# Performance work log

Measured on AMD Instinct MI355X. Metric: run time of the kernel, lower is better.

The kernel has to match this reference:

```python
import jax, jax.numpy as jnp
import numpy as np

N, C, H, W = 64, 64, 8, 8   # batch, channels (img_net_out_dim), feature-map HxW
E = 256                      # ques_rnn_hidden_dim
G = 512                      # rn_g_dim
FD = 512                     # rn_f_dim
GIN = 2 * (C + 2) + E        # g-MLP input dim = 388
NUM_CLASSES = 2


def _lin(key, din, dout):
    # kaiming-uniform-like init for a Linear stored as (in, out)
    bound = float(np.sqrt(6.0 / din))
    w = jax.random.uniform(key, (din, dout), minval=-bound, maxval=bound, dtype=jnp.float32)
    b = jnp.zeros((dout,), dtype=jnp.float32)
    return w, b


def setup_inputs() -> dict:
    key = jax.random.key(0)
    ks = jax.random.split(key, 9)
    img = jax.random.normal(ks[0], (N, C, H, W), dtype=jnp.float32)
    ques = jax.random.normal(ks[1], (N, E), dtype=jnp.float32)
    g_w1, g_b1 = _lin(ks[2], GIN, G)
    g_w2, g_b2 = _lin(ks[3], G, G)
    g_w3, g_b3 = _lin(ks[4], G, G)
    g_w4, g_b4 = _lin(ks[5], G, G)
    f_w1, f_b1 = _lin(ks[6], G, FD)
    f_w2, f_b2 = _lin(ks[7], FD, FD)
    f_w3, f_b3 = _lin(ks[8], FD, NUM_CLASSES)
    return dict(img=img, ques=ques,
                g_w1=g_w1, g_b1=g_b1, g_w2=g_w2, g_b2=g_b2,
                g_w3=g_w3, g_b3=g_b3, g_w4=g_w4, g_b4=g_b4,
                f_w1=f_w1, f_b1=f_b1, f_w2=f_w2, f_b2=f_b2,
                f_w3=f_w3, f_b3=f_b3)


def _img_to_pairs(img, ques):
    # img: (n, c, h, w), ques: (n, e) -> pairs: (n, hw*hw, 2*(c+2)+e)
    n, c, h, w = img.shape
    hw = h * w
    cells = img.reshape(n, c, hw)
    idx = jnp.arange(hw)
    loc = jnp.stack([idx // w, idx % w], axis=0).astype(img.dtype)  # (2, hw)
    cells = jnp.concatenate([cells, jnp.broadcast_to(loc[None], (n, 2, hw))], axis=1)
    feats = cells.transpose(0, 2, 1)  # (n, hw, c+2)
    fdim = feats.shape[-1]
    one = jnp.broadcast_to(feats[:, :, None, :], (n, hw, hw, fdim))   # object i
    two = jnp.broadcast_to(feats[:, None, :, :], (n, hw, hw, fdim))   # object j
    q = jnp.broadcast_to(ques[:, None, None, :], (n, hw, hw, ques.shape[-1]))
    return jnp.concatenate([one, two, q], axis=-1).reshape(n, hw * hw, -1)


def reference(img, ques, g_w1, g_b1, g_w2, g_b2, g_w3, g_b3, g_w4, g_b4,
              f_w1, f_b1, f_w2, f_b2, f_w3, f_b3):
    pairs = _img_to_pairs(img, ques)                      # (N, HW^2, GIN)
    hdd = jax.nn.relu(pairs @ g_w1 + g_b1)                # shared g-MLP over all pairs
    hdd = jax.nn.relu(hdd @ g_w2 + g_b2)
    hdd = jax.nn.relu(hdd @ g_w3 + g_b3)
    hdd = jax.nn.relu(hdd @ g_w4 + g_b4)
    context = hdd.mean(axis=1)                            # (N, G)
    z = jax.nn.relu(context @ f_w1 + f_b1)                # f-MLP (dropout = identity in eval)
    z = jax.nn.relu(z @ f_w2 + f_b2)
    scores = z @ f_w3 + f_b3                              # (N, 2)
    return jax.nn.log_softmax(scores, axis=1)
```

## Files before the change

### kernel.cpp

```cpp
#include <hip/hip_runtime.h>

typedef unsigned short u16;
typedef unsigned int u32;
typedef _Float16 f16;

using half8 = __attribute__((ext_vector_type(8))) _Float16;
using f32x4 = __attribute__((ext_vector_type(4))) float;
using f32x16 = __attribute__((ext_vector_type(16))) float;

__global__ __launch_bounds__(512) void prep_p12(const float* __restrict__ img,
                                                const float* __restrict__ gw1,
                                                float* __restrict__ P1,
                                                f16* __restrict__ P2h) {
    const int blk = blockIdx.x;
    const int n = blk >> 3;
    const int c0 = (blk & 7) * 8;
    const int t = threadIdx.x;
    __shared__ float feats[8][68];
    for (int idx = t; idx < 8 * 66; idx += 512) {
        int rr = idx / 66, cc = idx % 66, cell = c0 + rr;
        float v;
        if (cc < 64)       v = img[((size_t)(n * 64 + cc)) * 64 + cell];
        else if (cc == 64) v = (float)(cell >> 3);
        else               v = (float)(cell & 7);
        feats[rr][cc] = v;
    }
    __syncthreads();
    const int g = t;
    float a1[8], a2[8];
#pragma unroll
    for (int r = 0; r < 8; ++r) { a1[r] = 0.f; a2[r] = 0.f; }
    for (int c = 0; c < 66; ++c) {
        float wa = gw1[(size_t)c * 512 + g];
        float wb = gw1[(size_t)(66 + c) * 512 + g];
#pragma unroll
        for (int r = 0; r < 8; ++r) {
            a1[r] += feats[r][c] * wa;
            a2[r] += feats[r][c] * wb;
        }
    }
#pragma unroll
    for (int r = 0; r < 8; ++r) {
        P1[((size_t)(n * 64 + c0 + r)) * 512 + g] = a1[r];
        P2h[((size_t)(n * 64 + c0 + r)) * 512 + g] = (f16)a2[r];
    }
}

__global__ __launch_bounds__(512) void prep_q2(const float* __restrict__ ques,
                                               const float* __restrict__ gw1,
                                               const float* __restrict__ gb1,
                                               const float* __restrict__ P1,
                                               f16* __restrict__ P1h,
                                               float* __restrict__ Ctx) {
    const int n = blockIdx.x;
    const int t = threadIdx.x;
    __shared__ float q[256];
    if (t < 256) q[t] = ques[(size_t)n * 256 + t];
    __syncthreads();
    float acc = gb1[t];
    for (int e = 0; e < 256; ++e)
        acc += q[e] * gw1[(size_t)(132 + e) * 512 + t];
    const float* src = P1 + (((size_t)(n * 64)) << 9) + t;
    f16* dst = P1h + (((size_t)(n * 64)) << 9) + t;
    for (int r = 0; r < 64; ++r)
        dst[(size_t)r * 512] = (f16)(src[(size_t)r * 512] + acc);
    Ctx[(size_t)n * 512 + t] = 0.f;
}

__global__ void transpose_w(const float* __restrict__ W2, const float* __restrict__ W3,
                            const float* __restrict__ W4, f16* __restrict__ T2,
                            f16* __restrict__ T3, f16* __restrict__ T4) {
    const int L = blockIdx.z;
    const float* W = (L == 0) ? W2 : ((L == 1) ? W3 : W4);
    f16* T = (L == 0) ? T2 : ((L == 1) ? T3 : T4);
    __shared__ float tile[32][33];
    const int bx = blockIdx.x * 32;
    const int by = blockIdx.y * 32;
    const int tx = threadIdx.x, ty = threadIdx.y;
    for (int r = ty; r < 32; r += 8)
        tile[r][tx] = W[(size_t)(by + r) * 512 + bx + tx];
    __syncthreads();
    for (int r = ty; r < 32; r += 8)
        T[(size_t)(bx + r) * 512 + by + tx] = (f16)tile[tx][r];
}

__global__ __launch_bounds__(512, 2) void fused_g234(
    const f16* __restrict__ P1h, const f16* __restrict__ P2h,
    const f16* __restrict__ T2, const f16* __restrict__ T3,
    const f16* __restrict__ T4, const float* __restrict__ gb2,
    const float* __restrict__ gb3, const float* __restrict__ gb4,
    float* __restrict__ Ctx) {
    const int tid = threadIdx.x;
    const int lane = tid & 63;
    const int lane31 = lane & 31;
    const int khalf = lane >> 5;
    const int wv = tid >> 6;
    const int b = blockIdx.x;
    const int nb = b >> 5;
    const int i0 = (b & 31) * 2;

    __shared__ alignas(16) f16 H[128 * 512];

    const f16* P1b = P1h + (((size_t)(nb * 64 + i0)) << 9);
    const f16* P2b = P2h + (((size_t)(nb * 64)) << 9);

    {
        const int k0 = lane * 8;
#pragma unroll
        for (int u = 0; u < 16; ++u) {
            int r = u * 8 + wv;
            half8 x = *(const half8*)(P1b + (((size_t)(r >> 6)) << 9) + k0);
            half8 y = *(const half8*)(P2b + (((size_t)(r & 63)) << 9) + k0);
            half8 s = x + y;
            s = __builtin_elementwise_max(s, (half8)(f16)0.f);
            *(half8*)&H[r * 512 + (k0 ^ ((wv & 7) << 3))] = s;
        }
    }
    __syncthreads();

    f32x16 acc[4][2];
#pragma unroll
    for (int mi = 0; mi < 4; ++mi)
#pragma unroll
        for (int ni = 0; ni < 2; ++ni)
#pragma unroll
            for (int r = 0; r < 16; ++r)
                acc[mi][ni][r] = 0.f;

    auto loadB = [&](const f16* __restrict__ T, int ks, int ni) -> half8 {
        int col = wv * 64 + ni * 32 + lane31;
        return *(const half8*)(T + (((size_t)col) << 9) + ks * 16 + khalf * 8);
    };

    const int swz = (lane31 & 7) << 3;

    auto run_layer = [&](const f16* __restrict__ T) {
        half8 bfn[2];
#pragma unroll
        for (int ni = 0; ni < 2; ++ni) bfn[ni] = loadB(T, 0, ni);
#pragma unroll 4
        for (int ks = 0; ks < 32; ++ks) {
            half8 bf[2];
#pragma unroll
            for (int ni = 0; ni < 2; ++ni) bf[ni] = bfn[ni];
#pragma unroll
            for (int ni = 0; ni < 2; ++ni) bfn[ni] = loadB(T, (ks + 1) & 31, ni);
            const int koff = (ks * 16 + khalf * 8) ^ swz;
            half8 af[4];
#pragma unroll
            for (int mi = 0; mi < 4; ++mi)
                af[mi] = *(const half8*)&H[(mi * 32 + lane31) * 512 + koff];
#pragma unroll
            for (int mi = 0; mi < 4; ++mi)
#pragma unroll
                for (int ni = 0; ni < 2; ++ni)
                    acc[mi][ni] = __builtin_amdgcn_mfma_f32_32x32x16_f16(
                        af[mi], bf[ni], acc[mi][ni], 0, 0, 0);
        }
    };

    auto writeback = [&](const float* __restrict__ bias) {
        float bb[2];
#pragma unroll
        for (int ni = 0; ni < 2; ++ni)
            bb[ni] = bias[wv * 64 + ni * 32 + lane31];
        __syncthreads();
#pragma unroll
        for (int mi = 0; mi < 4; ++mi) {
#pragma unroll
            for (int ni = 0; ni < 2; ++ni) {
                int col = wv * 64 + ni * 32 + lane31;
#pragma unroll
                for (int r = 0; r < 16; ++r) {
                    int row = mi * 32 + (r & 3) + 4 * khalf + 8 * (r >> 2);
                    float v = fmaxf(acc[mi][ni][r] + bb[ni], 0.f);
                    H[row * 512 + (col ^ ((row & 7) << 3))] = (f16)v;
                    acc[mi][ni][r] = 0.f;
                }
            }
        }
        __syncthreads();
    };

    run_layer(T2);
    writeback(gb2);
    run_layer(T3);
    writeback(gb3);
    run_layer(T4);

#pragma unroll
    for (int ni = 0; ni < 2; ++ni) {
        int col = wv * 64 + ni * 32 + lane31;
        float bb = gb4[col];
        float s = 0.f;
#pragma unroll
        for (int mi = 0; mi < 4; ++mi)
#pragma unroll
            for (int r = 0; r < 16; ++r)
                s += fmaxf(acc[mi][ni][r] + bb, 0.f);
        s += __shfl_xor(s, 32, 64);
        if (khalf == 0)
            atomicAdd(&Ctx[(((size_t)nb) << 9) + col], s);
    }
}

__global__ __launch_bounds__(512) void fmlp_layer(
    const float* __restrict__ In, const float* __restrict__ Wt,
    const float* __restrict__ bias, float* __restrict__ Out, float scale) {
    const int n = blockIdx.x, cs = blockIdx.y;
    const int t = threadIdx.x;
    const int col = cs * 64 + (t & 63);
    const int seg = t >> 6;
    __shared__ float a[512];
    __shared__ float red[512];
    a[t] = In[(size_t)n * 512 + t] * scale;
    __syncthreads();
    float p = 0.f;
#pragma unroll 8
    for (int i = seg * 64; i < seg * 64 + 64; ++i)
        p += a[i] * Wt[(size_t)i * 512 + col];
    red[t] = p;
    __syncthreads();
    if (t < 64) {
        float v = bias[col];
#pragma unroll
        for (int sg = 0; sg < 8; ++sg) v += red[sg * 64 + t];
        Out[(size_t)n * 512 + cs * 64 + t] = fmaxf(v, 0.f);
    }
}

__global__ __launch_bounds__(64) void fmlp_out(
    const float* __restrict__ A2, const float* __restrict__ fw3,
    const float* __restrict__ fb3, float* __restrict__ out) {
    const int n = blockIdx.x;
    const int lane = threadIdx.x;
    float s0 = 0.f, s1 = 0.f;
    for (int i = lane; i < 512; i += 64) {
        float v = A2[(size_t)n * 512 + i];
        s0 += v * fw3[i * 2];
        s1 += v * fw3[i * 2 + 1];
    }
#pragma unroll
    for (int d = 1; d < 64; d <<= 1) {
        s0 += __shfl_xor(s0, d, 64);
        s1 += __shfl_xor(s1, d, 64);
    }
    if (lane == 0) {
        s0 += fb3[0];
        s1 += fb3[1];
        float m = fmaxf(s0, s1);
        float l = logf(expf(s0 - m) + expf(s1 - m)) + m;
        out[n * 2 + 0] = s0 - l;
        out[n * 2 + 1] = s1 - l;
    }
}

extern "C" void kernel_launch(void* const* d_in, const int* in_sizes, int n_in,
                              void* d_out, int out_size, void* d_ws, size_t ws_size,
                              hipStream_t stream) {
    const float* img  = (const float*)d_in[0];
    const float* ques = (const float*)d_in[1];
    const float* gw1  = (const float*)d_in[2];
    const float* gb1  = (const float*)d_in[3];
    const float* gw2  = (const float*)d_in[4];
    const float* gb2  = (const float*)d_in[5];
    const float* gw3  = (const float*)d_in[6];
    const float* gb3  = (const float*)d_in[7];
    const float* gw4  = (const float*)d_in[8];
    const float* gb4  = (const float*)d_in[9];
    const float* fw1  = (const float*)d_in[10];
    const float* fb1  = (const float*)d_in[11];
    const float* fw2  = (const float*)d_in[12];
    const float* fb2  = (const float*)d_in[13];
    const float* fw3  = (const float*)d_in[14];
    const float* fb3  = (const float*)d_in[15];

    char* ws = (char*)d_ws;
    size_t off = 0;
    float* P1  = (float*)(ws + off); off += (size_t)4096 * 512 * 4;
    f16* P1h = (f16*)(ws + off); off += (size_t)4096 * 512 * 2;
    f16* P2h = (f16*)(ws + off); off += (size_t)4096 * 512 * 2;
    float* Ctx = (float*)(ws + off); off += (size_t)64 * 512 * 4;
    float* Z1  = (float*)(ws + off); off += (size_t)64 * 512 * 4;
    float* Z2  = (float*)(ws + off); off += (size_t)64 * 512 * 4;
    f16* T2 = (f16*)(ws + off); off += (size_t)512 * 512 * 2;
    f16* T3 = (f16*)(ws + off); off += (size_t)512 * 512 * 2;
    f16* T4 = (f16*)(ws + off); off += (size_t)512 * 512 * 2;

    prep_p12<<<512, 512, 0, stream>>>(img, gw1, P1, P2h);
    prep_q2<<<64, 512, 0, stream>>>(ques, gw1, gb1, P1, P1h, Ctx);
    transpose_w<<<dim3(16, 16, 3), dim3(32, 8), 0, stream>>>(gw2, gw3, gw4, T2, T3, T4);

    fused_g234<<<2048, 512, 0, stream>>>(P1h, P2h, T2, T3, T4, gb2, gb3, gb4, Ctx);

    fmlp_layer<<<dim3(64, 8), 512, 0, stream>>>(Ctx, fw1, fb1, Z1, 1.0f / 4096.0f);
    fmlp_layer<<<dim3(64, 8), 512, 0, stream>>>(Z1, fw2, fb2, Z2, 1.0f);
    fmlp_out<<<64, 64, 0, stream>>>(Z2, fw3, fb3, (float*)d_out);
}
```

Measured before the change: 563.8 us.

## Retile fused g-MLP waves to 2x4 layout with double-buffered A/B fragment loads

Changes the per-wave output tile from 128 rows x 64 columns to 64 rows x 128 columns, arranging the 8 waves as a 2x4 grid. Each wave now reads half as many A fragments from LDS per k-step but twice as many B fragments from global memory. The k-loop is restructured into an explicit ping-pong of A and B fragment registers so that loads for the next step are issued while MFMAs run on the current one. s_setprio is raised around the MFMA groups. The aim is lower LDS traffic and better overlap of loads with MFMAs, at the cost of more global and L2 weight reads and more live registers.

```diff
diff --git a/kernel.cpp b/kernel.cpp
--- a/kernel.cpp
+++ b/kernel.cpp
@@ -95,6 +95,8 @@
     const int lane31 = lane & 31;
     const int khalf = lane >> 5;
     const int wv = tid >> 6;
+    const int wm = wv >> 2;
+    const int wn = wv & 3;
     const int b = blockIdx.x;
     const int nb = b >> 5;
     const int i0 = (b & 31) * 2;
@@ -118,61 +120,73 @@
     }
     __syncthreads();
 
-    f32x16 acc[4][2];
-#pragma unroll
-    for (int mi = 0; mi < 4; ++mi)
-#pragma unroll
-        for (int ni = 0; ni < 2; ++ni)
+    f32x16 acc[2][4];
+#pragma unroll
+    for (int mi = 0; mi < 2; ++mi)
+#pragma unroll
+        for (int ni = 0; ni < 4; ++ni)
 #pragma unroll
             for (int r = 0; r < 16; ++r)
                 acc[mi][ni][r] = 0.f;
 
-    auto loadB = [&](const f16* __restrict__ T, int ks, int ni) -> half8 {
-        int col = wv * 64 + ni * 32 + lane31;
-        return *(const half8*)(T + (((size_t)col) << 9) + ks * 16 + khalf * 8);
-    };
-
-    const int swz = (lane31 & 7) << 3;
+    const int rbase0 = (wm * 64 + lane31) * 512;
+    const int rbase1 = (wm * 64 + 32 + lane31) * 512;
+    const int kxor = ((khalf << 3) ^ ((lane31 & 7) << 3));
+
+    auto ldsA = [&](half8& a0, half8& a1, int ks) {
+        const int koff = (ks << 4) ^ kxor;
+        a0 = *(const half8*)&H[rbase0 + koff];
+        a1 = *(const half8*)&H[rbase1 + koff];
+    };
+    auto ldB = [&](half8 (&bf)[4], const f16* __restrict__ T, int ks) {
+        const f16* p = T + (((size_t)(wn * 128 + lane31)) << 9) + ks * 16 + khalf * 8;
+#pragma unroll
+        for (int ni = 0; ni < 4; ++ni)
+            bf[ni] = *(const half8*)(p + ((size_t)ni << 14));
+    };
+    auto mfma8 = [&](half8& a0, half8& a1, half8 (&bf)[4]) {
+        __builtin_amdgcn_s_setprio(1);
+#pragma unroll
+        for (int ni = 0; ni < 4; ++ni)
+            acc[0][ni] = __builtin_amdgcn_mfma_f32_32x32x16_f16(
+                a0, bf[ni], acc[0][ni], 0, 0, 0);
+#pragma unroll
+        for (int ni = 0; ni < 4; ++ni)
+            acc[1][ni] = __builtin_amdgcn_mfma_f32_32x32x16_f16(
+                a1, bf[ni], acc[1][ni], 0, 0, 0);
+        __builtin_amdgcn_s_setprio(0);
+    };
 
     auto run_layer = [&](const f16* __restrict__ T) {
-        half8 bfn[2];
-#pragma unroll
-        for (int ni = 0; ni < 2; ++ni) bfn[ni] = loadB(T, 0, ni);
-#pragma unroll 4
-        for (int ks = 0; ks < 32; ++ks) {
-            half8 bf[2];
-#pragma unroll
-            for (int ni = 0; ni < 2; ++ni) bf[ni] = bfn[ni];
-#pragma unroll
-            for (int ni = 0; ni < 2; ++ni) bfn[ni] = loadB(T, (ks + 1) & 31, ni);
-            const int koff = (ks * 16 + khalf * 8) ^ swz;
-            half8 af[4];
-#pragma unroll
-            for (int mi = 0; mi < 4; ++mi)
-                af[mi] = *(const half8*)&H[(mi * 32 + lane31) * 512 + koff];
-#pragma unroll
-            for (int mi = 0; mi < 4; ++mi)
-#pragma unroll
-                for (int ni = 0; ni < 2; ++ni)
-                    acc[mi][ni] = __builtin_amdgcn_mfma_f32_32x32x16_f16(
-                        af[mi], bf[ni], acc[mi][ni], 0, 0, 0);
+        half8 a0A, a1A, a0B, a1B, bfA[4], bfB[4];
+        ldsA(a0A, a1A, 0);
+        ldB(bfA, T, 0);
+        for (int ks = 0; ks < 32; ks += 2) {
+            ldsA(a0B, a1B, ks + 1);
+            ldB(bfB, T, ks + 1);
+            mfma8(a0A, a1A, bfA);
+            if (ks + 2 < 32) {
+                ldsA(a0A, a1A, ks + 2);
+                ldB(bfA, T, ks + 2);
+            }
+            mfma8(a0B, a1B, bfB);
         }
     };
 
     auto writeback = [&](const float* __restrict__ bias) {
-        float bb[2];
-#pragma unroll
-        for (int ni = 0; ni < 2; ++ni)
-            bb[ni] = bias[wv * 64 + ni * 32 + lane31];
+        float bb[4];
+#pragma unroll
+        for (int ni = 0; ni < 4; ++ni)
+            bb[ni] = bias[wn * 128 + ni * 32 + lane31];
         __syncthreads();
 #pragma unroll
-        for (int mi = 0; mi < 4; ++mi) {
-#pragma unroll
-            for (int ni = 0; ni < 2; ++ni) {
-                int col = wv * 64 + ni * 32 + lane31;
+        for (int mi = 0; mi < 2; ++mi) {
+#pragma unroll
+            for (int ni = 0; ni < 4; ++ni) {
+                const int col = wn * 128 + ni * 32 + lane31;
 #pragma unroll
                 for (int r = 0; r < 16; ++r) {
-                    int row = mi * 32 + (r & 3) + 4 * khalf + 8 * (r >> 2);
+                    const int row = wm * 64 + mi * 32 + (r & 3) + 4 * khalf + 8 * (r >> 2);
                     float v = fmaxf(acc[mi][ni][r] + bb[ni], 0.f);
                     H[row * 512 + (col ^ ((row & 7) << 3))] = (f16)v;
                     acc[mi][ni][r] = 0.f;
@@ -189,12 +203,12 @@
     run_layer(T4);
 
 #pragma unroll
-    for (int ni = 0; ni < 2; ++ni) {
-        int col = wv * 64 + ni * 32 + lane31;
+    for (int ni = 0; ni < 4; ++ni) {
+        const int col = wn * 128 + ni * 32 + lane31;
         float bb = gb4[col];
         float s = 0.f;
 #pragma unroll
-        for (int mi = 0; mi < 4; ++mi)
+        for (int mi = 0; mi < 2; ++mi)
 #pragma unroll
             for (int r = 0; r < 16; ++r)
                 s += fmaxf(acc[mi][ni][r] + bb, 0.f);
```

Measured after the change: 905.1 us. +60.5%, slower.

## Pre-pack B weights into MFMA fragment layout and double-buffer operand loads

Applied to the files above, without the earlier changes.

The weight transpose now writes the fp16 weights in a packed k-block layout (16-wide k chunks, split by k-half, 8 contiguous values per column), so each lane's B fragment load is contiguous across lanes and coalesced instead of strided by 512 elements. The inner GEMM loop becomes explicitly double-buffered: LDS A fragments and global B fragments for the next k-step are loaded while the MFMAs for the current step issue. The MFMA bursts are wrapped in s_setprio to favour matrix issue. This costs more live registers, which could reduce occupancy or cause spills under the 2-blocks-per-CU launch bound.

```diff
diff --git a/kernel.cpp b/kernel.cpp
--- a/kernel.cpp
+++ b/kernel.cpp
@@ -80,8 +80,11 @@
     for (int r = ty; r < 32; r += 8)
         tile[r][tx] = W[(size_t)(by + r) * 512 + bx + tx];
     __syncthreads();
-    for (int r = ty; r < 32; r += 8)
-        T[(size_t)(bx + r) * 512 + by + tx] = (f16)tile[tx][r];
+    for (int r = ty; r < 32; r += 8) {
+        const int n = bx + r, k = by + tx;
+        T[(size_t)(k >> 4) * 8192 + ((k >> 3) & 1) * 4096 + n * 8 + (k & 7)] =
+            (f16)tile[tx][r];
+    }
 }
 
 __global__ __launch_bounds__(512, 2) void fused_g234(
@@ -127,35 +130,44 @@
             for (int r = 0; r < 16; ++r)
                 acc[mi][ni][r] = 0.f;
 
-    auto loadB = [&](const f16* __restrict__ T, int ks, int ni) -> half8 {
-        int col = wv * 64 + ni * 32 + lane31;
-        return *(const half8*)(T + (((size_t)col) << 9) + ks * 16 + khalf * 8);
-    };
-
     const int swz = (lane31 & 7) << 3;
 
+    auto ldsA = [&](half8 (&a)[4], int ks) {
+        const int koff = ((ks << 4) | (khalf << 3)) ^ swz;
+#pragma unroll
+        for (int mi = 0; mi < 4; ++mi)
+            a[mi] = *(const half8*)&H[(mi * 32 + lane31) * 512 + koff];
+    };
+    auto ldB = [&](half8 (&bf)[2], const f16* __restrict__ T, int ks) {
+        const f16* p = T + ks * 8192 + khalf * 4096 + (wv * 64 + lane31) * 8;
+#pragma unroll
+        for (int ni = 0; ni < 2; ++ni)
+            bf[ni] = *(const half8*)(p + ni * 256);
+    };
+    auto mfma8 = [&](half8 (&a)[4], half8 (&bf)[2]) {
+        __builtin_amdgcn_s_setprio(1);
+#pragma unroll
+        for (int mi = 0; mi < 4; ++mi)
+#pragma unroll
+            for (int ni = 0; ni < 2; ++ni)
+                acc[mi][ni] = __builtin_amdgcn_mfma_f32_32x32x16_f16(
+                    a[mi], bf[ni], acc[mi][ni], 0, 0, 0);
+        __builtin_amdgcn_s_setprio(0);
+    };
+
     auto run_layer = [&](const f16* __restrict__ T) {
-        half8 bfn[2];
-#pragma unroll
-        for (int ni = 0; ni < 2; ++ni) bfn[ni] = loadB(T, 0, ni);
-#pragma unroll 4
-        for (int ks = 0; ks < 32; ++ks) {
-            half8 bf[2];
-#pragma unroll
-            for (int ni = 0; ni < 2; ++ni) bf[ni] = bfn[ni];
-#pragma unroll
-            for (int ni = 0; ni < 2; ++ni) bfn[ni] = loadB(T, (ks + 1) & 31, ni);
-            const int koff = (ks * 16 + khalf * 8) ^ swz;
-            half8 af[4];
-#pragma unroll
-            for (int mi = 0; mi < 4; ++mi)
-                af[mi] = *(const half8*)&H[(mi * 32 + lane31) * 512 + koff];
-#pragma unroll
-            for (int mi = 0; mi < 4; ++mi)
-#pragma unroll
-                for (int ni = 0; ni < 2; ++ni)
-                    acc[mi][ni] = __builtin_amdgcn_mfma_f32_32x32x16_f16(
-                        af[mi], bf[ni], acc[mi][ni], 0, 0, 0);
+        half8 aA[4], aB[4], bA[2], bB[2];
+        ldsA(aA, 0);
+        ldB(bA, T, 0);
+        for (int ks = 0; ks < 32; ks += 2) {
+            ldsA(aB, ks + 1);
+            ldB(bB, T, ks + 1);
+            mfma8(aA, bA);
+            if (ks + 2 < 32) {
+                ldsA(aA, ks + 2);
+                ldB(bA, T, ks + 2);
+            }
+            mfma8(aB, bB);
         }
     };
 
@@ -169,10 +181,10 @@
         for (int mi = 0; mi < 4; ++mi) {
 #pragma unroll
             for (int ni = 0; ni < 2; ++ni) {
-                int col = wv * 64 + ni * 32 + lane31;
+                const int col = wv * 64 + ni * 32 + lane31;
 #pragma unroll
                 for (int r = 0; r < 16; ++r) {
-                    int row = mi * 32 + (r & 3) + 4 * khalf + 8 * (r >> 2);
+                    const int row = mi * 32 + (r & 3) + 4 * khalf + 8 * (r >> 2);
                     float v = fmaxf(acc[mi][ni][r] + bb[ni], 0.f);
                     H[row * 512 + (col ^ ((row & 7) << 3))] = (f16)v;
                     acc[mi][ni][r] = 0.f;
@@ -190,7 +202,7 @@
 
 #pragma unroll
     for (int ni = 0; ni < 2; ++ni) {
-        int col = wv * 64 + ni * 32 + lane31;
+        const int col = wv * 64 + ni * 32 + lane31;
         float bb = gb4[col];
         float s = 0.f;
 #pragma unroll
```

Result: slower. 720.2 us (+27.7%).
